# Optimization experiments

Hardware: AMD Instinct MI355X
Metric: run time of the kernel (lower is better)

Reference implementation:

```python
import jax, jax.numpy as jnp
import numpy as np

HEADS = 4
K = 3  # neighborhood kernel size
EPS = 1e-5


def _nbr_idx(dim, k):
    # NATTEN semantics: window start clamped so the full k-window stays in-bounds.
    i = jnp.arange(dim)
    start = jnp.clip(i - k // 2, 0, dim - k)
    return start[:, None] + jnp.arange(k)[None, :]  # [dim, k]


def _gather_windows(t, ix, iy, iz):
    # t: [B, X, Y, Z, n, c] -> [B, X, Y, Z, K^3, n, c]
    t = t[:, ix]                 # [B, X, k, Y, Z, n, c]
    t = t[:, :, :, iy]           # [B, X, k, Y, k, Z, n, c]
    t = t[:, :, :, :, :, iz]     # [B, X, k, Y, k, Z, k, n, c]
    t = t.transpose(0, 1, 3, 5, 2, 4, 6, 7, 8)  # [B,X,Y,Z,k,k,k,n,c]
    B, X, Y, Z = t.shape[0], t.shape[1], t.shape[2], t.shape[3]
    return t.reshape(B, X, Y, Z, K * K * K, HEADS, -1)


def setup_inputs() -> dict:
    key = jax.random.key(0)
    k1, k2, k3 = jax.random.split(key, 3)
    C = 128
    x = jax.random.normal(k1, (1, C, 32, 32, 32), dtype=jnp.float32)
    ln_gamma = jnp.ones((C,), jnp.float32)
    ln_beta = jnp.zeros((C,), jnp.float32)
    qkv_w = jax.random.normal(k2, (3 * C, C), dtype=jnp.float32) * 0.02
    qkv_b = jnp.zeros((3 * C,), jnp.float32)
    proj_w = jax.random.normal(k3, (C, C), dtype=jnp.float32) * 0.02
    proj_b = jnp.zeros((C,), jnp.float32)
    return {"x": x, "ln_gamma": ln_gamma, "ln_beta": ln_beta,
            "qkv_w": qkv_w, "qkv_b": qkv_b, "proj_w": proj_w, "proj_b": proj_b}


def reference(x, ln_gamma, ln_beta, qkv_w, qkv_b, proj_w, proj_b):
    B, C, X, Y, Z = x.shape
    hd = C // HEADS
    scale = hd ** -0.5

    # permute to channels-last + LayerNorm over C
    h = x.transpose(0, 2, 3, 4, 1)  # [B,X,Y,Z,C]
    mu = jnp.mean(h, axis=-1, keepdims=True)
    var = jnp.mean(jnp.square(h - mu), axis=-1, keepdims=True)
    h = (h - mu) * jax.lax.rsqrt(var + EPS) * ln_gamma + ln_beta

    # QKV projection
    qkv = h @ qkv_w.T + qkv_b                     # [B,X,Y,Z,3C]
    q, k, v = jnp.split(qkv, 3, axis=-1)
    q = q.reshape(B, X, Y, Z, HEADS, hd)
    k = k.reshape(B, X, Y, Z, HEADS, hd)
    v = v.reshape(B, X, Y, Z, HEADS, hd)

    ix, iy, iz = _nbr_idx(X, K), _nbr_idx(Y, K), _nbr_idx(Z, K)
    k_win = _gather_windows(k, ix, iy, iz)  # [B,X,Y,Z,27,n,hd]
    v_win = _gather_windows(v, ix, iy, iz)

    attn = jnp.einsum('bxyznc,bxyzknc->bxyznk', q * scale, k_win)
    attn = jax.nn.softmax(attn, axis=-1)
    out = jnp.einsum('bxyznk,bxyzknc->bxyznc', attn, v_win)
    out = out.reshape(B, X, Y, Z, C)

    out = out @ proj_w.T + proj_b                 # output projection
    return out.transpose(0, 4, 1, 2, 3) + x      # residual, channels-first
```

## Files before the change

kernel.cpp:

```cpp
#include <hip/hip_runtime.h>

#define N_VOX 32768
#define CCH 128
#define EPSV 1e-5f

typedef __attribute__((ext_vector_type(8))) short bfrag;
typedef __attribute__((ext_vector_type(4))) float ffrag;
typedef __attribute__((ext_vector_type(2))) unsigned int u32x2;

__device__ __forceinline__ float bf2f(unsigned short u) {
    union { unsigned int i; float f; } c; c.i = ((unsigned int)u) << 16; return c.f;
}
__device__ __forceinline__ unsigned short f2bf(float f) {
    union { float f; unsigned int i; } c; c.f = f;
    unsigned int i = c.i;
    return (unsigned short)((i + 0x7FFFu + ((i >> 16) & 1u)) >> 16);
}

__global__ __launch_bounds__(256) void ln_kernel(const float* __restrict__ x,
                                                 const float* __restrict__ gamma,
                                                 const float* __restrict__ beta,
                                                 unsigned short* __restrict__ h) {
    __shared__ float xs[128 * 65];
    __shared__ float g[128], b[128];
    __shared__ float ps[256], pq[256];
    __shared__ float muS[64], rsS[64];
    int t = threadIdx.x;
    int v0 = blockIdx.x * 64;
    if (t < 128) { g[t] = gamma[t]; b[t] = beta[t]; }
    int vv = t & 63, cq = t >> 6;
    for (int cb = 0; cb < 32; cb++) {
        int c = cb * 4 + cq;
        xs[c * 65 + vv] = x[(size_t)c * N_VOX + v0 + vv];
    }
    __syncthreads();
    float s = 0.f, sq = 0.f;
    for (int i = 0; i < 32; i++) {
        float val = xs[(cq * 32 + i) * 65 + vv];
        s += val; sq += val * val;
    }
    ps[t] = s; pq[t] = sq;
    __syncthreads();
    if (t < 64) {
        float S = ps[t] + ps[t + 64] + ps[t + 128] + ps[t + 192];
        float Q = pq[t] + pq[t + 64] + pq[t + 128] + pq[t + 192];
        float mu = S * (1.0f / 128.0f);
        float var = Q * (1.0f / 128.0f) - mu * mu;
        muS[t] = mu; rsS[t] = rsqrtf(var + EPSV);
    }
    __syncthreads();
    int c8 = t & 15;
    for (int pass = 0; pass < 4; pass++) {
        int v = pass * 16 + (t >> 4);
        float mu = muS[v], rs = rsS[v];
        union { unsigned short u[8]; uint4 q; } pk;
        #pragma unroll
        for (int i = 0; i < 8; i++) {
            int c = c8 * 8 + i;
            float val = (xs[c * 65 + v] - mu) * rs * g[c] + b[c];
            pk.u[i] = f2bf(val);
        }
        *(uint4*)&h[(size_t)(v0 + v) * 128 + c8 * 8] = pk.q;
    }
}

__global__ __launch_bounds__(256) void qkv_gemm(const unsigned short* __restrict__ h,
                                                const float* __restrict__ w,
                                                const float* __restrict__ bias,
                                                unsigned short* __restrict__ qkv) {
    __shared__ __align__(16) unsigned short a_s[64 * 136];
    __shared__ __align__(16) unsigned short b_s[64 * 136];
    int t = threadIdx.x;
    int m0 = blockIdx.x * 64, o0 = blockIdx.y * 64;
    {
        int r4 = t >> 4, c8 = t & 15;
        #pragma unroll
        for (int pass = 0; pass < 4; pass++) {
            int r = pass * 16 + r4;
            *(uint4*)&a_s[r * 136 + c8 * 8] =
                *(const uint4*)&h[(size_t)(m0 + r) * 128 + c8 * 8];
            float4 w0 = *(const float4*)&w[(size_t)(o0 + r) * 128 + c8 * 8];
            float4 w1 = *(const float4*)&w[(size_t)(o0 + r) * 128 + c8 * 8 + 4];
            union { unsigned short u[8]; uint4 q; } pk;
            pk.u[0] = f2bf(w0.x); pk.u[1] = f2bf(w0.y);
            pk.u[2] = f2bf(w0.z); pk.u[3] = f2bf(w0.w);
            pk.u[4] = f2bf(w1.x); pk.u[5] = f2bf(w1.y);
            pk.u[6] = f2bf(w1.z); pk.u[7] = f2bf(w1.w);
            *(uint4*)&b_s[r * 136 + c8 * 8] = pk.q;
        }
    }
    __syncthreads();
    int wvi = t >> 6, lane = t & 63, m = lane & 15, quad = lane >> 4;
    ffrag acc[4] = {ffrag{0,0,0,0}, ffrag{0,0,0,0}, ffrag{0,0,0,0}, ffrag{0,0,0,0}};
    #pragma unroll
    for (int kk = 0; kk < 4; kk++) {
        bfrag a = *(bfrag*)&a_s[(wvi * 16 + m) * 136 + kk * 32 + quad * 8];
        #pragma unroll
        for (int nt = 0; nt < 4; nt++) {
            bfrag bb = *(bfrag*)&b_s[(nt * 16 + m) * 136 + kk * 32 + quad * 8];
            acc[nt] = __builtin_amdgcn_mfma_f32_16x16x32_bf16(a, bb, acc[nt], 0, 0, 0);
        }
    }
    bool isq = (o0 < 128);
    #pragma unroll
    for (int nt = 0; nt < 4; nt++) {
        int o = o0 + nt * 16 + m;
        float bs = bias[o];
        int sec = o >> 7;
        int oc = o & 127;
        unsigned short* dst = qkv + (size_t)sec * ((size_t)N_VOX * 128);
        #pragma unroll
        for (int r = 0; r < 4; r++) {
            int vg = m0 + wvi * 16 + quad * 4 + r;
            float val = acc[nt][r] + bs;
            if (isq) val *= 0.17677669529663687f;
            dst[(size_t)vg * 128 + oc] = f2bf(val);
        }
    }
}

#define VT_STRIDE 188
__global__ __launch_bounds__(256) void attn_kernel(const unsigned short* __restrict__ qb,
                                                   const unsigned short* __restrict__ kb,
                                                   const unsigned short* __restrict__ vb,
                                                   unsigned short* __restrict__ ob) {
    __shared__ unsigned int vjtab[176];
    __shared__ __align__(16) unsigned short vt[4][32 * VT_STRIDE];

    int t = threadIdx.x;
    int bidx = blockIdx.x;
    int zh = bidx & 1, yy = (bidx >> 1) & 31, xx = bidx >> 6;
    int z0 = zh << 4;
    int sx = min(max(xx - 1, 0), 29);
    int sy = min(max(yy - 1, 0), 29);
    int zr0 = min(max(z0 - 1, 0), 14);
    int vox0 = (xx << 10) + (yy << 5) + z0;

    if (t < 176) {
        int r = t < 162 ? t : 161;
        int rxy = r / 18;
        int rzv = r - rxy * 18;
        int ax = rxy / 3;
        int by = rxy - ax * 3;
        vjtab[t] = (unsigned)(((sx + ax) << 10) + ((sy + by) << 5) + (zr0 + rzv));
    }
    __syncthreads();

    int wave = t >> 6, lane = t & 63;
    int hq = lane >> 4;
    int m = lane & 15;
    int ch0 = wave * 32;

    unsigned short* vts = &vt[wave][0];
    {
        const int cp = m;
        #pragma unroll
        for (int u = 0; u < 11; u++) {
            int rb = u * 16 + hq * 4;
            unsigned int j0 = vjtab[rb + 0];
            unsigned int j1 = vjtab[rb + 1];
            unsigned int j2 = vjtab[rb + 2];
            unsigned int j3 = vjtab[rb + 3];
            unsigned int d0 = *(const unsigned int*)&vb[(size_t)j0 * 128 + ch0 + cp * 2];
            unsigned int d1 = *(const unsigned int*)&vb[(size_t)j1 * 128 + ch0 + cp * 2];
            unsigned int d2 = *(const unsigned int*)&vb[(size_t)j2 * 128 + ch0 + cp * 2];
            unsigned int d3 = *(const unsigned int*)&vb[(size_t)j3 * 128 + ch0 + cp * 2];
            if (u == 10) {
                if (rb + 0 >= 162) d0 = 0u;
                if (rb + 1 >= 162) d1 = 0u;
                if (rb + 2 >= 162) d2 = 0u;
                if (rb + 3 >= 162) d3 = 0u;
            }
            unsigned int lo01 = __builtin_amdgcn_perm(d1, d0, 0x05040100u);
            unsigned int lo23 = __builtin_amdgcn_perm(d3, d2, 0x05040100u);
            unsigned int hi01 = __builtin_amdgcn_perm(d1, d0, 0x07060302u);
            unsigned int hi23 = __builtin_amdgcn_perm(d3, d2, 0x07060302u);
            u32x2 wlo; wlo.x = lo01; wlo.y = lo23;
            u32x2 whi; whi.x = hi01; whi.y = hi23;
            *(u32x2*)&vts[(2 * cp) * VT_STRIDE + rb] = wlo;
            *(u32x2*)&vts[(2 * cp + 1) * VT_STRIDE + rb] = whi;
        }
    }

    bfrag qf = *(const bfrag*)&qb[(size_t)(vox0 + m) * 128 + ch0 + hq * 8];
    ffrag s[11];
    #pragma unroll
    for (int f = 0; f < 11; f++) {
        unsigned int vj = vjtab[f * 16 + m];
        bfrag kf = *(const bfrag*)&kb[(size_t)vj * 128 + ch0 + hq * 8];
        s[f] = __builtin_amdgcn_mfma_f32_16x16x32_bf16(kf, qf, ffrag{0,0,0,0}, 0, 0, 0);
    }

    int zv = z0 + m;
    int szv = min(max(zv - 1, 0), 29);
    unsigned int wz = (unsigned int)(szv - zr0);
    unsigned int rz = 4u * (unsigned int)hq;
    float mx = -1e30f;
    #pragma unroll
    for (int f = 0; f < 11; f++) {
        #pragma unroll
        for (int i = 0; i < 4; i++) {
            unsigned int ri = rz + (unsigned int)i;
            ri = min(ri, ri - 18u);
            bool valid = (ri - wz) <= 2u;
            if (f == 10) valid = valid && ((4 * hq + i) < 2);
            float sv = valid ? s[f][i] : -1e30f;
            s[f][i] = sv;
            mx = fmaxf(mx, sv);
        }
        rz = min(rz + 16u, rz - 2u);
    }
    mx = fmaxf(mx, __shfl_xor(mx, 16));
    mx = fmaxf(mx, __shfl_xor(mx, 32));
    float sum = 0.f;
    #pragma unroll
    for (int f = 0; f < 11; f++) {
        #pragma unroll
        for (int i = 0; i < 4; i++) {
            float p = __expf(s[f][i] - mx);
            s[f][i] = p;
            sum += p;
        }
    }
    sum += __shfl_xor(sum, 16);
    sum += __shfl_xor(sum, 32);
    float inv = 1.0f / sum;

    ffrag acc0 = ffrag{0,0,0,0};
    ffrag acc1 = ffrag{0,0,0,0};
    const unsigned short* ab = &vt[wave][m * VT_STRIDE + hq * 4];
    #pragma unroll
    for (int f = 0; f < 11; f++) {
        unsigned int plo, phi;
        asm("v_cvt_pk_bf16_f32 %0, %1, %2" : "=v"(plo) : "v"(s[f][0]), "v"(s[f][1]));
        asm("v_cvt_pk_bf16_f32 %0, %1, %2" : "=v"(phi) : "v"(s[f][2]), "v"(s[f][3]));
        u32x2 pb; pb.x = plo; pb.y = phi;
        u32x2 av0 = *(const u32x2*)&ab[f * 16];
        u32x2 av1 = *(const u32x2*)&ab[16 * VT_STRIDE + f * 16];
        asm("v_mfma_f32_16x16x16_bf16 %0, %1, %2, %0" : "+v"(acc0) : "v"(av0), "v"(pb));
        asm("v_mfma_f32_16x16x16_bf16 %0, %1, %2, %0" : "+v"(acc1) : "v"(av1), "v"(pb));
    }

    size_t obase = (size_t)(vox0 + m) * 128 + ch0 + hq * 4;
    {
        float a0 = acc0[0] * inv, a1 = acc0[1] * inv, a2 = acc0[2] * inv, a3 = acc0[3] * inv;
        unsigned int p0, p1;
        asm("v_cvt_pk_bf16_f32 %0, %1, %2" : "=v"(p0) : "v"(a0), "v"(a1));
        asm("v_cvt_pk_bf16_f32 %0, %1, %2" : "=v"(p1) : "v"(a2), "v"(a3));
        u32x2 ov; ov.x = p0; ov.y = p1;
        *(u32x2*)&ob[obase] = ov;
    }
    {
        float a0 = acc1[0] * inv, a1 = acc1[1] * inv, a2 = acc1[2] * inv, a3 = acc1[3] * inv;
        unsigned int p0, p1;
        asm("v_cvt_pk_bf16_f32 %0, %1, %2" : "=v"(p0) : "v"(a0), "v"(a1));
        asm("v_cvt_pk_bf16_f32 %0, %1, %2" : "=v"(p1) : "v"(a2), "v"(a3));
        u32x2 ov; ov.x = p0; ov.y = p1;
        *(u32x2*)&ob[obase + 16] = ov;
    }
}

__global__ __launch_bounds__(256) void proj_gemm(const unsigned short* __restrict__ a,
                                                 const float* __restrict__ w,
                                                 const float* __restrict__ bias,
                                                 const float* __restrict__ xres,
                                                 float* __restrict__ out) {
    __shared__ __align__(16) unsigned short a_s[64 * 136];
    __shared__ __align__(16) unsigned short b_s[64 * 136];
    int t = threadIdx.x;
    int m0 = blockIdx.x * 64, o0 = blockIdx.y * 64;
    {
        int r4 = t >> 4, c8 = t & 15;
        #pragma unroll
        for (int pass = 0; pass < 4; pass++) {
            int r = pass * 16 + r4;
            *(uint4*)&a_s[r * 136 + c8 * 8] =
                *(const uint4*)&a[(size_t)(m0 + r) * 128 + c8 * 8];
            float4 w0 = *(const float4*)&w[(size_t)(o0 + r) * 128 + c8 * 8];
            float4 w1 = *(const float4*)&w[(size_t)(o0 + r) * 128 + c8 * 8 + 4];
            union { unsigned short u[8]; uint4 q; } pk;
            pk.u[0] = f2bf(w0.x); pk.u[1] = f2bf(w0.y);
            pk.u[2] = f2bf(w0.z); pk.u[3] = f2bf(w0.w);
            pk.u[4] = f2bf(w1.x); pk.u[5] = f2bf(w1.y);
            pk.u[6] = f2bf(w1.z); pk.u[7] = f2bf(w1.w);
            *(uint4*)&b_s[r * 136 + c8 * 8] = pk.q;
        }
    }
    __syncthreads();
    int wvi = t >> 6, lane = t & 63, m = lane & 15, quad = lane >> 4;
    ffrag acc[4] = {ffrag{0,0,0,0}, ffrag{0,0,0,0}, ffrag{0,0,0,0}, ffrag{0,0,0,0}};
    #pragma unroll
    for (int kk = 0; kk < 4; kk++) {
        bfrag av = *(bfrag*)&a_s[(wvi * 16 + m) * 136 + kk * 32 + quad * 8];
        #pragma unroll
        for (int nt = 0; nt < 4; nt++) {
            bfrag bb = *(bfrag*)&b_s[(nt * 16 + m) * 136 + kk * 32 + quad * 8];
            acc[nt] = __builtin_amdgcn_mfma_f32_16x16x32_bf16(av, bb, acc[nt], 0, 0, 0);
        }
    }
    #pragma unroll
    for (int nt = 0; nt < 4; nt++) {
        int o = o0 + nt * 16 + m;
        float bs = bias[o];
        int vg = m0 + wvi * 16 + quad * 4;
        float4 r = *(const float4*)&xres[(size_t)o * N_VOX + vg];
        float4 ov;
        ov.x = acc[nt][0] + bs + r.x;
        ov.y = acc[nt][1] + bs + r.y;
        ov.z = acc[nt][2] + bs + r.z;
        ov.w = acc[nt][3] + bs + r.w;
        *(float4*)&out[(size_t)o * N_VOX + vg] = ov;
    }
}

extern "C" void kernel_launch(void* const* d_in, const int* in_sizes, int n_in,
                              void* d_out, int out_size, void* d_ws, size_t ws_size,
                              hipStream_t stream) {
    const float* x      = (const float*)d_in[0];
    const float* gamma  = (const float*)d_in[1];
    const float* beta   = (const float*)d_in[2];
    const float* qkv_w  = (const float*)d_in[3];
    const float* qkv_b  = (const float*)d_in[4];
    const float* proj_w = (const float*)d_in[5];
    const float* proj_b = (const float*)d_in[6];
    float* out = (float*)d_out;

    unsigned short* h    = (unsigned short*)d_ws;
    unsigned short* qkv  = (unsigned short*)((char*)d_ws + (8u << 20));
    unsigned short* attn = h;

    hipLaunchKernelGGL(ln_kernel, dim3(512), dim3(256), 0, stream, x, gamma, beta, h);
    hipLaunchKernelGGL(qkv_gemm, dim3(512, 6), dim3(256), 0, stream, h, qkv_w, qkv_b, qkv);
    const unsigned short* qb = qkv;
    const unsigned short* kb = qkv + (size_t)N_VOX * 128;
    const unsigned short* vb = qkv + (size_t)2 * N_VOX * 128;
    hipLaunchKernelGGL(attn_kernel, dim3(2048), dim3(256), 0, stream, qb, kb, vb, attn);
    hipLaunchKernelGGL(proj_gemm, dim3(512, 2), dim3(256), 0, stream, attn, proj_w, proj_b, x, out);
}
```

Measured before the change: 122.7 us.

## Fuse LayerNorm into QKV GEMM and output projection into attention kernel

```diff
diff --git a/kernel.cpp b/kernel.cpp
--- a/kernel.cpp
+++ b/kernel.cpp
@@ -17,27 +17,28 @@
     return (unsigned short)((i + 0x7FFFu + ((i >> 16) & 1u)) >> 16);
 }
 
-__global__ __launch_bounds__(256) void ln_kernel(const float* __restrict__ x,
-                                                 const float* __restrict__ gamma,
-                                                 const float* __restrict__ beta,
-                                                 unsigned short* __restrict__ h) {
-    __shared__ float xs[128 * 65];
-    __shared__ float g[128], b[128];
+__global__ __launch_bounds__(256) void ln_qkv(const float* __restrict__ x,
+                                              const float* __restrict__ gamma,
+                                              const float* __restrict__ beta,
+                                              const float* __restrict__ w,
+                                              const float* __restrict__ bias,
+                                              unsigned short* __restrict__ qkv) {
+    __shared__ __align__(16) unsigned short a_s[64 * 136];
+    __shared__ __align__(16) unsigned short b_s[64 * 136];
     __shared__ float ps[256], pq[256];
     __shared__ float muS[64], rsS[64];
+    __shared__ float g[128], bta[128];
     int t = threadIdx.x;
-    int v0 = blockIdx.x * 64;
-    if (t < 128) { g[t] = gamma[t]; b[t] = beta[t]; }
-    int vv = t & 63, cq = t >> 6;
-    for (int cb = 0; cb < 32; cb++) {
-        int c = cb * 4 + cq;
-        xs[c * 65 + vv] = x[(size_t)c * N_VOX + v0 + vv];
-    }
-    __syncthreads();
+    int og = blockIdx.x;
+    int v0 = blockIdx.y * 64;
+    if (t < 128) { g[t] = gamma[t]; bta[t] = beta[t]; }
+    int cq = t >> 6, v = t & 63;
+    float xr[32];
     float s = 0.f, sq = 0.f;
+    #pragma unroll
     for (int i = 0; i < 32; i++) {
-        float val = xs[(cq * 32 + i) * 65 + vv];
-        s += val; sq += val * val;
+        float val = x[(size_t)(cq * 32 + i) * N_VOX + v0 + v];
+        xr[i] = val; s += val; sq += val * val;
     }
     ps[t] = s; pq[t] = sq;
     __syncthreads();
@@ -49,83 +50,83 @@
         muS[t] = mu; rsS[t] = rsqrtf(var + EPSV);
     }
     __syncthreads();
-    int c8 = t & 15;
-    for (int pass = 0; pass < 4; pass++) {
-        int v = pass * 16 + (t >> 4);
+    {
         float mu = muS[v], rs = rsS[v];
-        union { unsigned short u[8]; uint4 q; } pk;
-        #pragma unroll
-        for (int i = 0; i < 8; i++) {
-            int c = c8 * 8 + i;
-            float val = (xs[c * 65 + v] - mu) * rs * g[c] + b[c];
-            pk.u[i] = f2bf(val);
-        }
-        *(uint4*)&h[(size_t)(v0 + v) * 128 + c8 * 8] = pk.q;
-    }
-}
-
-__global__ __launch_bounds__(256) void qkv_gemm(const unsigned short* __restrict__ h,
-                                                const float* __restrict__ w,
-                                                const float* __restrict__ bias,
-                                                unsigned short* __restrict__ qkv) {
-    __shared__ __align__(16) unsigned short a_s[64 * 136];
-    __shared__ __align__(16) unsigned short b_s[64 * 136];
-    int t = threadIdx.x;
-    int m0 = blockIdx.x * 64, o0 = blockIdx.y * 64;
-    {
-        int r4 = t >> 4, c8 = t & 15;
-        #pragma unroll
-        for (int pass = 0; pass < 4; pass++) {
-            int r = pass * 16 + r4;
-            *(uint4*)&a_s[r * 136 + c8 * 8] =
-                *(const uint4*)&h[(size_t)(m0 + r) * 128 + c8 * 8];
-            float4 w0 = *(const float4*)&w[(size_t)(o0 + r) * 128 + c8 * 8];
-            float4 w1 = *(const float4*)&w[(size_t)(o0 + r) * 128 + c8 * 8 + 4];
+        #pragma unroll
+        for (int i8 = 0; i8 < 4; i8++) {
             union { unsigned short u[8]; uint4 q; } pk;
-            pk.u[0] = f2bf(w0.x); pk.u[1] = f2bf(w0.y);
-            pk.u[2] = f2bf(w0.z); pk.u[3] = f2bf(w0.w);
-            pk.u[4] = f2bf(w1.x); pk.u[5] = f2bf(w1.y);
-            pk.u[6] = f2bf(w1.z); pk.u[7] = f2bf(w1.w);
-            *(uint4*)&b_s[r * 136 + c8 * 8] = pk.q;
-        }
-    }
-    __syncthreads();
-    int wvi = t >> 6, lane = t & 63, m = lane & 15, quad = lane >> 4;
-    ffrag acc[4] = {ffrag{0,0,0,0}, ffrag{0,0,0,0}, ffrag{0,0,0,0}, ffrag{0,0,0,0}};
-    #pragma unroll
-    for (int kk = 0; kk < 4; kk++) {
-        bfrag a = *(bfrag*)&a_s[(wvi * 16 + m) * 136 + kk * 32 + quad * 8];
+            #pragma unroll
+            for (int k = 0; k < 8; k++) {
+                int c = cq * 32 + i8 * 8 + k;
+                pk.u[k] = f2bf((xr[i8 * 8 + k] - mu) * rs * g[c] + bta[c]);
+            }
+            *(uint4*)&a_s[v * 136 + cq * 32 + i8 * 8] = pk.q;
+        }
+    }
+    __syncthreads();
+    int lane = t & 63, wvi = t >> 6, m = lane & 15, quad = lane >> 4;
+    bfrag areg[4];
+    #pragma unroll
+    for (int kk = 0; kk < 4; kk++)
+        areg[kk] = *(bfrag*)&a_s[(wvi * 16 + m) * 136 + kk * 32 + quad * 8];
+    for (int t0 = 0; t0 < 3; t0++) {
+        int o0 = og * 192 + t0 * 64;
+        {
+            int r4 = t >> 4, c8 = t & 15;
+            #pragma unroll
+            for (int pass = 0; pass < 4; pass++) {
+                int r = pass * 16 + r4;
+                float4 w0 = *(const float4*)&w[(size_t)(o0 + r) * 128 + c8 * 8];
+                float4 w1 = *(const float4*)&w[(size_t)(o0 + r) * 128 + c8 * 8 + 4];
+                union { unsigned short u[8]; uint4 q; } pk;
+                pk.u[0] = f2bf(w0.x); pk.u[1] = f2bf(w0.y);
+                pk.u[2] = f2bf(w0.z); pk.u[3] = f2bf(w0.w);
+                pk.u[4] = f2bf(w1.x); pk.u[5] = f2bf(w1.y);
+                pk.u[6] = f2bf(w1.z); pk.u[7] = f2bf(w1.w);
+                *(uint4*)&b_s[r * 136 + c8 * 8] = pk.q;
+            }
+        }
+        __syncthreads();
+        ffrag acc[4] = {ffrag{0,0,0,0}, ffrag{0,0,0,0}, ffrag{0,0,0,0}, ffrag{0,0,0,0}};
+        #pragma unroll
+        for (int kk = 0; kk < 4; kk++) {
+            #pragma unroll
+            for (int nt = 0; nt < 4; nt++) {
+                bfrag bb = *(bfrag*)&b_s[(nt * 16 + m) * 136 + kk * 32 + quad * 8];
+                acc[nt] = __builtin_amdgcn_mfma_f32_16x16x32_bf16(areg[kk], bb, acc[nt], 0, 0, 0);
+            }
+        }
+        bool isq = (o0 < 128);
         #pragma unroll
         for (int nt = 0; nt < 4; nt++) {
-            bfrag bb = *(bfrag*)&b_s[(nt * 16 + m) * 136 + kk * 32 + quad * 8];
-            acc[nt] = __builtin_amdgcn_mfma_f32_16x16x32_bf16(a, bb, acc[nt], 0, 0, 0);
-        }
-    }
-    bool isq = (o0 < 128);
-    #pragma unroll
-    for (int nt = 0; nt < 4; nt++) {
-        int o = o0 + nt * 16 + m;
-        float bs = bias[o];
-        int sec = o >> 7;
-        int oc = o & 127;
-        unsigned short* dst = qkv + (size_t)sec * ((size_t)N_VOX * 128);
-        #pragma unroll
-        for (int r = 0; r < 4; r++) {
-            int vg = m0 + wvi * 16 + quad * 4 + r;
-            float val = acc[nt][r] + bs;
-            if (isq) val *= 0.17677669529663687f;
-            dst[(size_t)vg * 128 + oc] = f2bf(val);
-        }
+            int o = o0 + nt * 16 + m;
+            float bs = bias[o];
+            int sec = o >> 7;
+            int oc = o & 127;
+            unsigned short* dst = qkv + (size_t)sec * ((size_t)N_VOX * 128);
+            #pragma unroll
+            for (int r = 0; r < 4; r++) {
+                int vg = v0 + wvi * 16 + quad * 4 + r;
+                float val = acc[nt][r] + bs;
+                if (isq) val *= 0.17677669529663687f;
+                dst[(size_t)vg * 128 + oc] = f2bf(val);
+            }
+        }
+        __syncthreads();
     }
 }
 
 #define VT_STRIDE 188
-__global__ __launch_bounds__(256) void attn_kernel(const unsigned short* __restrict__ qb,
-                                                   const unsigned short* __restrict__ kb,
-                                                   const unsigned short* __restrict__ vb,
-                                                   unsigned short* __restrict__ ob) {
+__global__ __launch_bounds__(256) void attn_proj(const unsigned short* __restrict__ qb,
+                                                 const unsigned short* __restrict__ kb,
+                                                 const unsigned short* __restrict__ vb,
+                                                 const float* __restrict__ pw,
+                                                 const float* __restrict__ pbias,
+                                                 const float* __restrict__ xres,
+                                                 float* __restrict__ out) {
     __shared__ unsigned int vjtab[176];
     __shared__ __align__(16) unsigned short vt[4][32 * VT_STRIDE];
+    unsigned int* os = (unsigned int*)&vt[0][0];
 
     int t = threadIdx.x;
     int bidx = blockIdx.x;
@@ -241,75 +242,54 @@
         asm("v_mfma_f32_16x16x16_bf16 %0, %1, %2, %0" : "+v"(acc1) : "v"(av1), "v"(pb));
     }
 
-    size_t obase = (size_t)(vox0 + m) * 128 + ch0 + hq * 4;
+    unsigned int af0, af1, af2, af3;
     {
         float a0 = acc0[0] * inv, a1 = acc0[1] * inv, a2 = acc0[2] * inv, a3 = acc0[3] * inv;
-        unsigned int p0, p1;
-        asm("v_cvt_pk_bf16_f32 %0, %1, %2" : "=v"(p0) : "v"(a0), "v"(a1));
-        asm("v_cvt_pk_bf16_f32 %0, %1, %2" : "=v"(p1) : "v"(a2), "v"(a3));
-        u32x2 ov; ov.x = p0; ov.y = p1;
-        *(u32x2*)&ob[obase] = ov;
-    }
+        asm("v_cvt_pk_bf16_f32 %0, %1, %2" : "=v"(af0) : "v"(a0), "v"(a1));
+        asm("v_cvt_pk_bf16_f32 %0, %1, %2" : "=v"(af1) : "v"(a2), "v"(a3));
+        float b0 = acc1[0] * inv, b1 = acc1[1] * inv, b2 = acc1[2] * inv, b3 = acc1[3] * inv;
+        asm("v_cvt_pk_bf16_f32 %0, %1, %2" : "=v"(af2) : "v"(b0), "v"(b1));
+        asm("v_cvt_pk_bf16_f32 %0, %1, %2" : "=v"(af3) : "v"(b2), "v"(b3));
+    }
+    __syncthreads();
     {
-        float a0 = acc1[0] * inv, a1 = acc1[1] * inv, a2 = acc1[2] * inv, a3 = acc1[3] * inv;
-        unsigned int p0, p1;
-        asm("v_cvt_pk_bf16_f32 %0, %1, %2" : "=v"(p0) : "v"(a0), "v"(a1));
-        asm("v_cvt_pk_bf16_f32 %0, %1, %2" : "=v"(p1) : "v"(a2), "v"(a3));
-        u32x2 ov; ov.x = p0; ov.y = p1;
-        *(u32x2*)&ob[obase + 16] = ov;
-    }
-}
-
-__global__ __launch_bounds__(256) void proj_gemm(const unsigned short* __restrict__ a,
-                                                 const float* __restrict__ w,
-                                                 const float* __restrict__ bias,
-                                                 const float* __restrict__ xres,
-                                                 float* __restrict__ out) {
-    __shared__ __align__(16) unsigned short a_s[64 * 136];
-    __shared__ __align__(16) unsigned short b_s[64 * 136];
-    int t = threadIdx.x;
-    int m0 = blockIdx.x * 64, o0 = blockIdx.y * 64;
-    {
-        int r4 = t >> 4, c8 = t & 15;
-        #pragma unroll
-        for (int pass = 0; pass < 4; pass++) {
-            int r = pass * 16 + r4;
-            *(uint4*)&a_s[r * 136 + c8 * 8] =
-                *(const uint4*)&a[(size_t)(m0 + r) * 128 + c8 * 8];
-            float4 w0 = *(const float4*)&w[(size_t)(o0 + r) * 128 + c8 * 8];
-            float4 w1 = *(const float4*)&w[(size_t)(o0 + r) * 128 + c8 * 8 + 4];
-            union { unsigned short u[8]; uint4 q; } pk;
-            pk.u[0] = f2bf(w0.x); pk.u[1] = f2bf(w0.y);
-            pk.u[2] = f2bf(w0.z); pk.u[3] = f2bf(w0.w);
-            pk.u[4] = f2bf(w1.x); pk.u[5] = f2bf(w1.y);
-            pk.u[6] = f2bf(w1.z); pk.u[7] = f2bf(w1.w);
-            *(uint4*)&b_s[r * 136 + c8 * 8] = pk.q;
-        }
-    }
-    __syncthreads();
-    int wvi = t >> 6, lane = t & 63, m = lane & 15, quad = lane >> 4;
-    ffrag acc[4] = {ffrag{0,0,0,0}, ffrag{0,0,0,0}, ffrag{0,0,0,0}, ffrag{0,0,0,0}};
-    #pragma unroll
-    for (int kk = 0; kk < 4; kk++) {
-        bfrag av = *(bfrag*)&a_s[(wvi * 16 + m) * 136 + kk * 32 + quad * 8];
-        #pragma unroll
-        for (int nt = 0; nt < 4; nt++) {
-            bfrag bb = *(bfrag*)&b_s[(nt * 16 + m) * 136 + kk * 32 + quad * 8];
-            acc[nt] = __builtin_amdgcn_mfma_f32_16x16x32_bf16(av, bb, acc[nt], 0, 0, 0);
-        }
-    }
-    #pragma unroll
-    for (int nt = 0; nt < 4; nt++) {
-        int o = o0 + nt * 16 + m;
-        float bs = bias[o];
-        int vg = m0 + wvi * 16 + quad * 4;
-        float4 r = *(const float4*)&xres[(size_t)o * N_VOX + vg];
-        float4 ov;
-        ov.x = acc[nt][0] + bs + r.x;
-        ov.y = acc[nt][1] + bs + r.y;
-        ov.z = acc[nt][2] + bs + r.z;
-        ov.w = acc[nt][3] + bs + r.w;
-        *(float4*)&out[(size_t)o * N_VOX + vg] = ov;
+        unsigned int* osl = os + (wave * 64 + lane) * 6;
+        u32x2 w0; w0.x = af0; w0.y = af1;
+        u32x2 w1; w1.x = af2; w1.y = af3;
+        *(u32x2*)osl = w0;
+        *(u32x2*)(osl + 2) = w1;
+    }
+    __syncthreads();
+
+    ffrag pacc0 = ffrag{0,0,0,0};
+    ffrag pacc1 = ffrag{0,0,0,0};
+    int cA = wave * 32;
+    int cB = cA + 16;
+    #pragma unroll
+    for (int cb2 = 0; cb2 < 8; cb2++) {
+        int wsrc = cb2 >> 1, half = cb2 & 1;
+        u32x2 bfr = *(const u32x2*)(os + (wsrc * 64 + hq * 16 + m) * 6 + half * 2);
+        float4 wa = *(const float4*)&pw[(size_t)(cA + m) * 128 + cb2 * 16 + hq * 4];
+        float4 wb = *(const float4*)&pw[(size_t)(cB + m) * 128 + cb2 * 16 + hq * 4];
+        unsigned int a0, a1, b0, b1;
+        asm("v_cvt_pk_bf16_f32 %0, %1, %2" : "=v"(a0) : "v"(wa.x), "v"(wa.y));
+        asm("v_cvt_pk_bf16_f32 %0, %1, %2" : "=v"(a1) : "v"(wa.z), "v"(wa.w));
+        asm("v_cvt_pk_bf16_f32 %0, %1, %2" : "=v"(b0) : "v"(wb.x), "v"(wb.y));
+        asm("v_cvt_pk_bf16_f32 %0, %1, %2" : "=v"(b1) : "v"(wb.z), "v"(wb.w));
+        u32x2 awA; awA.x = a0; awA.y = a1;
+        u32x2 awB; awB.x = b0; awB.y = b1;
+        asm("v_mfma_f32_16x16x16_bf16 %0, %1, %2, %0" : "+v"(pacc0) : "v"(awA), "v"(bfr));
+        asm("v_mfma_f32_16x16x16_bf16 %0, %1, %2, %0" : "+v"(pacc1) : "v"(awB), "v"(bfr));
+    }
+
+    #pragma unroll
+    for (int r = 0; r < 4; r++) {
+        int c0 = cA + hq * 4 + r;
+        int c1 = cB + hq * 4 + r;
+        size_t i0 = (size_t)c0 * N_VOX + vox0 + m;
+        size_t i1 = (size_t)c1 * N_VOX + vox0 + m;
+        out[i0] = pacc0[r] + pbias[c0] + xres[i0];
+        out[i1] = pacc1[r] + pbias[c1] + xres[i1];
     }
 }
 
@@ -325,15 +305,13 @@
     const float* proj_b = (const float*)d_in[6];
     float* out = (float*)d_out;
 
-    unsigned short* h    = (unsigned short*)d_ws;
-    unsigned short* qkv  = (unsigned short*)((char*)d_ws + (8u << 20));
-    unsigned short* attn = h;
-
-    hipLaunchKernelGGL(ln_kernel, dim3(512), dim3(256), 0, stream, x, gamma, beta, h);
-    hipLaunchKernelGGL(qkv_gemm, dim3(512, 6), dim3(256), 0, stream, h, qkv_w, qkv_b, qkv);
+    unsigned short* qkv = (unsigned short*)d_ws;
+
+    hipLaunchKernelGGL(ln_qkv, dim3(2, 512), dim3(256), 0, stream,
+                       x, gamma, beta, qkv_w, qkv_b, qkv);
     const unsigned short* qb = qkv;
     const unsigned short* kb = qkv + (size_t)N_VOX * 128;
     const unsigned short* vb = qkv + (size_t)2 * N_VOX * 128;
-    hipLaunchKernelGGL(attn_kernel, dim3(2048), dim3(256), 0, stream, qb, kb, vb, attn);
-    hipLaunchKernelGGL(proj_gemm, dim3(512, 2), dim3(256), 0, stream, attn, proj_w, proj_b, x, out);
-}
+    hipLaunchKernelGGL(attn_proj, dim3(2048), dim3(256), 0, stream,
+                       qb, kb, vb, proj_w, proj_b, x, out);
+}
```

New measurement: 127.9 us. +4.3%, slower.

## Stage V tile in two halves to halve LDS; use hardware bf16 pack

Applied to the files above, without the earlier changes.

```diff
diff --git a/kernel.cpp b/kernel.cpp
--- a/kernel.cpp
+++ b/kernel.cpp
@@ -15,6 +15,11 @@
     union { float f; unsigned int i; } c; c.f = f;
     unsigned int i = c.i;
     return (unsigned short)((i + 0x7FFFu + ((i >> 16) & 1u)) >> 16);
+}
+__device__ __forceinline__ unsigned int cvtpk(float lo, float hi) {
+    unsigned int r;
+    asm("v_cvt_pk_bf16_f32 %0, %1, %2" : "=v"(r) : "v"(lo), "v"(hi));
+    return r;
 }
 
 __global__ __launch_bounds__(256) void ln_kernel(const float* __restrict__ x,
@@ -53,14 +58,18 @@
     for (int pass = 0; pass < 4; pass++) {
         int v = pass * 16 + (t >> 4);
         float mu = muS[v], rs = rsS[v];
-        union { unsigned short u[8]; uint4 q; } pk;
+        float val[8];
         #pragma unroll
         for (int i = 0; i < 8; i++) {
             int c = c8 * 8 + i;
-            float val = (xs[c * 65 + v] - mu) * rs * g[c] + b[c];
-            pk.u[i] = f2bf(val);
-        }
-        *(uint4*)&h[(size_t)(v0 + v) * 128 + c8 * 8] = pk.q;
+            val[i] = (xs[c * 65 + v] - mu) * rs * g[c] + b[c];
+        }
+        uint4 q;
+        q.x = cvtpk(val[0], val[1]);
+        q.y = cvtpk(val[2], val[3]);
+        q.z = cvtpk(val[4], val[5]);
+        q.w = cvtpk(val[6], val[7]);
+        *(uint4*)&h[(size_t)(v0 + v) * 128 + c8 * 8] = q;
     }
 }
 
@@ -81,12 +90,12 @@
                 *(const uint4*)&h[(size_t)(m0 + r) * 128 + c8 * 8];
             float4 w0 = *(const float4*)&w[(size_t)(o0 + r) * 128 + c8 * 8];
             float4 w1 = *(const float4*)&w[(size_t)(o0 + r) * 128 + c8 * 8 + 4];
-            union { unsigned short u[8]; uint4 q; } pk;
-            pk.u[0] = f2bf(w0.x); pk.u[1] = f2bf(w0.y);
-            pk.u[2] = f2bf(w0.z); pk.u[3] = f2bf(w0.w);
-            pk.u[4] = f2bf(w1.x); pk.u[5] = f2bf(w1.y);
-            pk.u[6] = f2bf(w1.z); pk.u[7] = f2bf(w1.w);
-            *(uint4*)&b_s[r * 136 + c8 * 8] = pk.q;
+            uint4 q;
+            q.x = cvtpk(w0.x, w0.y);
+            q.y = cvtpk(w0.z, w0.w);
+            q.z = cvtpk(w1.x, w1.y);
+            q.w = cvtpk(w1.z, w1.w);
+            *(uint4*)&b_s[r * 136 + c8 * 8] = q;
         }
     }
     __syncthreads();
@@ -119,7 +128,7 @@
     }
 }
 
-#define VT_STRIDE 188
+#define VT_STRIDE 100
 __global__ __launch_bounds__(256) void attn_kernel(const unsigned short* __restrict__ qb,
                                                    const unsigned short* __restrict__ kb,
                                                    const unsigned short* __restrict__ vb,
@@ -150,36 +159,28 @@
     int hq = lane >> 4;
     int m = lane & 15;
     int ch0 = wave * 32;
-
     unsigned short* vts = &vt[wave][0];
-    {
-        const int cp = m;
-        #pragma unroll
-        for (int u = 0; u < 11; u++) {
-            int rb = u * 16 + hq * 4;
-            unsigned int j0 = vjtab[rb + 0];
-            unsigned int j1 = vjtab[rb + 1];
-            unsigned int j2 = vjtab[rb + 2];
-            unsigned int j3 = vjtab[rb + 3];
-            unsigned int d0 = *(const unsigned int*)&vb[(size_t)j0 * 128 + ch0 + cp * 2];
-            unsigned int d1 = *(const unsigned int*)&vb[(size_t)j1 * 128 + ch0 + cp * 2];
-            unsigned int d2 = *(const unsigned int*)&vb[(size_t)j2 * 128 + ch0 + cp * 2];
-            unsigned int d3 = *(const unsigned int*)&vb[(size_t)j3 * 128 + ch0 + cp * 2];
-            if (u == 10) {
-                if (rb + 0 >= 162) d0 = 0u;
-                if (rb + 1 >= 162) d1 = 0u;
-                if (rb + 2 >= 162) d2 = 0u;
-                if (rb + 3 >= 162) d3 = 0u;
-            }
-            unsigned int lo01 = __builtin_amdgcn_perm(d1, d0, 0x05040100u);
-            unsigned int lo23 = __builtin_amdgcn_perm(d3, d2, 0x05040100u);
-            unsigned int hi01 = __builtin_amdgcn_perm(d1, d0, 0x07060302u);
-            unsigned int hi23 = __builtin_amdgcn_perm(d3, d2, 0x07060302u);
-            u32x2 wlo; wlo.x = lo01; wlo.y = lo23;
-            u32x2 whi; whi.x = hi01; whi.y = hi23;
-            *(u32x2*)&vts[(2 * cp) * VT_STRIDE + rb] = wlo;
-            *(u32x2*)&vts[(2 * cp + 1) * VT_STRIDE + rb] = whi;
-        }
+    const int cp = m;
+
+    #pragma unroll
+    for (int u = 0; u < 6; u++) {
+        int rb = u * 16 + hq * 4;
+        unsigned int j0 = vjtab[rb + 0];
+        unsigned int j1 = vjtab[rb + 1];
+        unsigned int j2 = vjtab[rb + 2];
+        unsigned int j3 = vjtab[rb + 3];
+        unsigned int d0 = *(const unsigned int*)&vb[(size_t)j0 * 128 + ch0 + cp * 2];
+        unsigned int d1 = *(const unsigned int*)&vb[(size_t)j1 * 128 + ch0 + cp * 2];
+        unsigned int d2 = *(const unsigned int*)&vb[(size_t)j2 * 128 + ch0 + cp * 2];
+        unsigned int d3 = *(const unsigned int*)&vb[(size_t)j3 * 128 + ch0 + cp * 2];
+        unsigned int lo01 = __builtin_amdgcn_perm(d1, d0, 0x05040100u);
+        unsigned int lo23 = __builtin_amdgcn_perm(d3, d2, 0x05040100u);
+        unsigned int hi01 = __builtin_amdgcn_perm(d1, d0, 0x07060302u);
+        unsigned int hi23 = __builtin_amdgcn_perm(d3, d2, 0x07060302u);
+        u32x2 wlo; wlo.x = lo01; wlo.y = lo23;
+        u32x2 whi; whi.x = hi01; whi.y = hi23;
+        *(u32x2*)&vts[(2 * cp) * VT_STRIDE + rb] = wlo;
+        *(u32x2*)&vts[(2 * cp + 1) * VT_STRIDE + rb] = whi;
     }
 
     bfrag qf = *(const bfrag*)&qb[(size_t)(vox0 + m) * 128 + ch0 + hq * 8];
@@ -230,32 +231,63 @@
     ffrag acc1 = ffrag{0,0,0,0};
     const unsigned short* ab = &vt[wave][m * VT_STRIDE + hq * 4];
     #pragma unroll
-    for (int f = 0; f < 11; f++) {
-        unsigned int plo, phi;
-        asm("v_cvt_pk_bf16_f32 %0, %1, %2" : "=v"(plo) : "v"(s[f][0]), "v"(s[f][1]));
-        asm("v_cvt_pk_bf16_f32 %0, %1, %2" : "=v"(phi) : "v"(s[f][2]), "v"(s[f][3]));
-        u32x2 pb; pb.x = plo; pb.y = phi;
+    for (int f = 0; f < 6; f++) {
+        u32x2 pb; pb.x = cvtpk(s[f][0], s[f][1]); pb.y = cvtpk(s[f][2], s[f][3]);
         u32x2 av0 = *(const u32x2*)&ab[f * 16];
         u32x2 av1 = *(const u32x2*)&ab[16 * VT_STRIDE + f * 16];
         asm("v_mfma_f32_16x16x16_bf16 %0, %1, %2, %0" : "+v"(acc0) : "v"(av0), "v"(pb));
         asm("v_mfma_f32_16x16x16_bf16 %0, %1, %2, %0" : "+v"(acc1) : "v"(av1), "v"(pb));
     }
 
+    #pragma unroll
+    for (int u = 6; u < 11; u++) {
+        int rb = u * 16 + hq * 4;
+        unsigned int j0 = vjtab[rb + 0];
+        unsigned int j1 = vjtab[rb + 1];
+        unsigned int j2 = vjtab[rb + 2];
+        unsigned int j3 = vjtab[rb + 3];
+        unsigned int d0 = *(const unsigned int*)&vb[(size_t)j0 * 128 + ch0 + cp * 2];
+        unsigned int d1 = *(const unsigned int*)&vb[(size_t)j1 * 128 + ch0 + cp * 2];
+        unsigned int d2 = *(const unsigned int*)&vb[(size_t)j2 * 128 + ch0 + cp * 2];
+        unsigned int d3 = *(const unsigned int*)&vb[(size_t)j3 * 128 + ch0 + cp * 2];
+        if (u == 10) {
+            if (rb + 0 >= 162) d0 = 0u;
+            if (rb + 1 >= 162) d1 = 0u;
+            if (rb + 2 >= 162) d2 = 0u;
+            if (rb + 3 >= 162) d3 = 0u;
+        }
+        unsigned int lo01 = __builtin_amdgcn_perm(d1, d0, 0x05040100u);
+        unsigned int lo23 = __builtin_amdgcn_perm(d3, d2, 0x05040100u);
+        unsigned int hi01 = __builtin_amdgcn_perm(d1, d0, 0x07060302u);
+        unsigned int hi23 = __builtin_amdgcn_perm(d3, d2, 0x07060302u);
+        u32x2 wlo; wlo.x = lo01; wlo.y = lo23;
+        u32x2 whi; whi.x = hi01; whi.y = hi23;
+        int lc = rb - 96;
+        *(u32x2*)&vts[(2 * cp) * VT_STRIDE + lc] = wlo;
+        *(u32x2*)&vts[(2 * cp + 1) * VT_STRIDE + lc] = whi;
+    }
+
+    #pragma unroll
+    for (int f = 6; f < 11; f++) {
+        u32x2 pb; pb.x = cvtpk(s[f][0], s[f][1]); pb.y = cvtpk(s[f][2], s[f][3]);
+        int lc = f * 16 - 96;
+        u32x2 av0 = *(const u32x2*)&ab[lc];
+        u32x2 av1 = *(const u32x2*)&ab[16 * VT_STRIDE + lc];
+        asm("v_mfma_f32_16x16x16_bf16 %0, %1, %2, %0" : "+v"(acc0) : "v"(av0), "v"(pb));
+        asm("v_mfma_f32_16x16x16_bf16 %0, %1, %2, %0" : "+v"(acc1) : "v"(av1), "v"(pb));
+    }
+
     size_t obase = (size_t)(vox0 + m) * 128 + ch0 + hq * 4;
     {
-        float a0 = acc0[0] * inv, a1 = acc0[1] * inv, a2 = acc0[2] * inv, a3 = acc0[3] * inv;
-        unsigned int p0, p1;
-        asm("v_cvt_pk_bf16_f32 %0, %1, %2" : "=v"(p0) : "v"(a0), "v"(a1));
-        asm("v_cvt_pk_bf16_f32 %0, %1, %2" : "=v"(p1) : "v"(a2), "v"(a3));
-        u32x2 ov; ov.x = p0; ov.y = p1;
+        u32x2 ov;
+        ov.x = cvtpk(acc0[0] * inv, acc0[1] * inv);
+        ov.y = cvtpk(acc0[2] * inv, acc0[3] * inv);
         *(u32x2*)&ob[obase] = ov;
     }
     {
-        float a0 = acc1[0] * inv, a1 = acc1[1] * inv, a2 = acc1[2] * inv, a3 = acc1[3] * inv;
-        unsigned int p0, p1;
-        asm("v_cvt_pk_bf16_f32 %0, %1, %2" : "=v"(p0) : "v"(a0), "v"(a1));
-        asm("v_cvt_pk_bf16_f32 %0, %1, %2" : "=v"(p1) : "v"(a2), "v"(a3));
-        u32x2 ov; ov.x = p0; ov.y = p1;
+        u32x2 ov;
+        ov.x = cvtpk(acc1[0] * inv, acc1[1] * inv);
+        ov.y = cvtpk(acc1[2] * inv, acc1[3] * inv);
         *(u32x2*)&ob[obase + 16] = ov;
     }
 }
@@ -278,12 +310,12 @@
                 *(const uint4*)&a[(size_t)(m0 + r) * 128 + c8 * 8];
             float4 w0 = *(const float4*)&w[(size_t)(o0 + r) * 128 + c8 * 8];
             float4 w1 = *(const float4*)&w[(size_t)(o0 + r) * 128 + c8 * 8 + 4];
-            union { unsigned short u[8]; uint4 q; } pk;
-            pk.u[0] = f2bf(w0.x); pk.u[1] = f2bf(w0.y);
-            pk.u[2] = f2bf(w0.z); pk.u[3] = f2bf(w0.w);
-            pk.u[4] = f2bf(w1.x); pk.u[5] = f2bf(w1.y);
-            pk.u[6] = f2bf(w1.z); pk.u[7] = f2bf(w1.w);
-            *(uint4*)&b_s[r * 136 + c8 * 8] = pk.q;
+            uint4 q;
+            q.x = cvtpk(w0.x, w0.y);
+            q.y = cvtpk(w0.z, w0.w);
+            q.z = cvtpk(w1.x, w1.y);
+            q.w = cvtpk(w1.z, w1.w);
+            *(uint4*)&b_s[r * 136 + c8 * 8] = q;
         }
     }
     __syncthreads();
```

Result: slower. 129.5 us (+5.6%).
